# Performance work log

Hardware: AMD Instinct MI355X
Metric: run time of the kernel (lower is better)

Reference implementation:

```python
import jax, jax.numpy as jnp
import numpy as np

NUM_HEADS = 6

def setup_inputs() -> dict:
    key = jax.random.key(0)
    k1, k2, k3, k4 = jax.random.split(key, 4)
    B, N, C = 8, 2048, 384
    x = jax.random.normal(k1, (B, N, C), dtype=jnp.float32)
    qkv_w = jax.random.normal(k2, (3 * C, C), dtype=jnp.float32) * (C ** -0.5)
    proj_w = jax.random.normal(k3, (C, C), dtype=jnp.float32) * (C ** -0.5)
    proj_b = jax.random.normal(k4, (C,), dtype=jnp.float32) * 0.01
    temperature = jnp.ones((NUM_HEADS, 1, 1), dtype=jnp.float32)
    return {"x": x, "qkv_w": qkv_w, "proj_w": proj_w, "proj_b": proj_b,
            "temperature": temperature}


def reference(x, qkv_w, proj_w, proj_b, temperature):
    B, N, C = x.shape
    H = NUM_HEADS
    Dh = C // H
    # qkv projection (no bias), split into q, k, v per head
    qkv = (x @ qkv_w.T).reshape(B, N, 3, H, Dh)
    qkv = jnp.transpose(qkv, (2, 0, 3, 1, 4))  # [3, B, H, N, Dh]
    q, k, v = qkv[0], qkv[1], qkv[2]
    # scores scaled by sqrt(C) (full dim, as in source), then learnable temperature
    attn = jnp.einsum('bhnd,bhmd->bhnm', q, k) / (C ** 0.5)
    attn = attn / temperature  # temperature: [H,1,1] broadcasts over B and N,N
    # diagonal (self-token) mask -> -inf before softmax
    diag = jnp.eye(N, dtype=bool)
    attn = jnp.where(diag, -jnp.inf, attn)
    attn = jax.nn.softmax(attn, axis=-1)
    # attend and merge heads
    out = jnp.einsum('bhnm,bhmd->bhnd', attn, v)
    out = jnp.transpose(out, (0, 2, 1, 3)).reshape(B, N, C)
    # output projection
    return out @ proj_w.T + proj_b
```

## Files before the change

kernel.cpp:

```cpp
#include <hip/hip_runtime.h>


using f32x4 = __attribute__((ext_vector_type(4))) float;
using s16x8 = __attribute__((ext_vector_type(8))) short;
using u16x4 = __attribute__((ext_vector_type(4))) unsigned short;
using u32x2 = __attribute__((ext_vector_type(2))) unsigned int;
using u32x4 = __attribute__((ext_vector_type(4))) unsigned int;
typedef unsigned short u16;
typedef unsigned int u32;

#define MFMA16(a, b, c) __builtin_amdgcn_mfma_f32_16x16x32_bf16(a, b, c, 0, 0, 0)
#define LOG2E 1.4426950408889634f
#define SQRTC 19.595917942265423f

__device__ __forceinline__ u16 f2bf(float f) {
  u32 u = __float_as_uint(f);
  u += 0x7fffu + ((u >> 16) & 1u);
  return (u16)(u >> 16);
}

__device__ __forceinline__ u32 cvtpk(float lo, float hi) {
  u32 r;
  asm("v_cvt_pk_bf16_f32 %0, %1, %2" : "=v"(r) : "v"(lo), "v"(hi));
  return r;
}

__device__ __forceinline__ float fexp2(float x) {
  float r;
  asm("v_exp_f32 %0, %1" : "=v"(r) : "v"(x));
  return r;
}

__device__ __forceinline__ void gld16(const void* g, void* l) {
  __builtin_amdgcn_global_load_lds((const __attribute__((address_space(1))) void*)g,
                                   (__attribute__((address_space(3))) void*)l, 16, 0, 0);
}

__global__ __launch_bounds__(256) void k_cvt2(const float* __restrict__ A,
                                              u16* __restrict__ Oa,
                                              const float* __restrict__ B,
                                              u16* __restrict__ Ob) {
  const int bid = blockIdx.x;
  const float* in;
  u16* out;
  size_t i;
  if (bid < 432) { in = A; out = Oa; i = (size_t)bid * 256 + threadIdx.x; }
  else           { in = B; out = Ob; i = (size_t)(bid - 432) * 256 + threadIdx.x; }
  f32x4 v = *(const f32x4*)(in + i * 4);
  u16x4 o;
  o[0] = f2bf(v[0]); o[1] = f2bf(v[1]); o[2] = f2bf(v[2]); o[3] = f2bf(v[3]);
  *(u16x4*)(out + i * 4) = o;
}

__global__ __launch_bounds__(256) void k_qkv(const float* __restrict__ X,
                                             const u16* __restrict__ W,
                                             const float* __restrict__ temp,
                                             u16* __restrict__ Qt,
                                             u16* __restrict__ Kb,
                                             u16* __restrict__ Vt) {
  __shared__ u16 As[2][128 * 32];
  __shared__ u16 Bs[2][128 * 32];
  const int tid = threadIdx.x, w = tid >> 6, l = tid & 63, lr = l & 15, lg = l >> 4;
  const int id = blockIdx.y * 9 + blockIdx.x;
  const int swz = (id & 7) * 144 + (id >> 3);
  const int tn = (swz % 9) * 128, tm = (swz / 9) * 128;
  const int wr = w >> 1, wc = w & 1;
  const int r0 = tid >> 2, c8 = (tid & 3) * 8;
  const int ar = tid >> 1, ac = (tid & 1) * 16;

  f32x4 acc[4][4] = {};
  f32x4 a4[4];

  auto issueA = [&](int kt) {
    const float* xp = X + (size_t)(tm + ar) * 384 + kt * 32 + ac;
    a4[0] = *(const f32x4*)(xp);
    a4[1] = *(const f32x4*)(xp + 4);
    a4[2] = *(const f32x4*)(xp + 8);
    a4[3] = *(const f32x4*)(xp + 12);
  };
  auto commitA = [&](int buf) {
    u32x4 h0, h1;
    h0[0] = cvtpk(a4[0][0], a4[0][1]); h0[1] = cvtpk(a4[0][2], a4[0][3]);
    h0[2] = cvtpk(a4[1][0], a4[1][1]); h0[3] = cvtpk(a4[1][2], a4[1][3]);
    h1[0] = cvtpk(a4[2][0], a4[2][1]); h1[1] = cvtpk(a4[2][2], a4[2][3]);
    h1[2] = cvtpk(a4[3][0], a4[3][1]); h1[3] = cvtpk(a4[3][2], a4[3][3]);
    *(u32x4*)&As[buf][ar * 32 + ac] = h0;
    *(u32x4*)&As[buf][ar * 32 + ac + 8] = h1;
  };
  auto stageB = [&](int buf, int kt) {
    const int k0 = kt * 32;
    char* db = (char*)(&Bs[buf][0]) + (w << 10);
    gld16(W + (size_t)(tn + r0) * 384 + k0 + c8, db);
    gld16(W + (size_t)(tn + 64 + r0) * 384 + k0 + c8, db + 4096);
  };

  issueA(0); stageB(0, 0); commitA(0);
  for (int kt = 0; kt < 12; ++kt) {
    __syncthreads();
    if (kt < 11) { issueA(kt + 1); stageB((kt + 1) & 1, kt + 1); }
    const int buf = kt & 1;
    s16x8 af[4], bfr[4];
    for (int mi = 0; mi < 4; mi++)
      af[mi] = *(const s16x8*)&As[buf][(wr * 64 + mi * 16 + lr) * 32 + lg * 8];
    for (int ni = 0; ni < 4; ni++)
      bfr[ni] = *(const s16x8*)&Bs[buf][(wc * 64 + ni * 16 + lr) * 32 + lg * 8];
    for (int mi = 0; mi < 4; mi++)
      for (int ni = 0; ni < 4; ni++)
        acc[mi][ni] = MFMA16(af[mi], bfr[ni], acc[mi][ni]);
    if (kt < 11) commitA((kt + 1) & 1);
  }

  const int which = (tn + wc * 64) / 384;
  const int bidx = (tm >> 11);
  for (int mi = 0; mi < 4; mi++)
    for (int ni = 0; ni < 4; ni++) {
      const int n = tn + wc * 64 + ni * 16 + lr;
      const int c = n - which * 384;
      const int h = c >> 6, d = c & 63;
      const size_t bh = (size_t)(bidx * 6 + h);
      if (which == 1) {
        for (int j = 0; j < 4; j++) {
          const int pos = (tm + wr * 64 + mi * 16 + lg * 4 + j) & 2047;
          Kb[(bh * 2048 + pos) * 64 + d] = f2bf(acc[mi][ni][j]);
        }
      } else {
        const float mult = (which == 0) ? (LOG2E / (SQRTC * temp[h])) : 1.0f;
        const int pos0 = (tm + wr * 64 + mi * 16 + lg * 4) & 2047;
        u16x4 vv;
        vv[0] = f2bf(acc[mi][ni][0] * mult); vv[1] = f2bf(acc[mi][ni][1] * mult);
        vv[2] = f2bf(acc[mi][ni][2] * mult); vv[3] = f2bf(acc[mi][ni][3] * mult);
        u16* dst = (which == 0) ? Qt : Vt;
        *(u16x4*)&dst[(bh * 64 + d) * 2048 + pos0] = vv;
      }
    }
}

#define LDSOFF(row, c16) (((row) * 128 + (c16) * 16) ^ (((row) & 7) << 4))

__global__ __launch_bounds__(256, 3) void k_attn(const u16* __restrict__ Qt,
                                                 const u16* __restrict__ Kb,
                                                 const u16* __restrict__ Vt,
                                                 u16* __restrict__ AO) {
  __shared__ u16 Ks[2][64 * 64];
  __shared__ u16 Vs[2][64 * 64];
  __shared__ u16 Ps[4][32 * 72];
  const int tid = threadIdx.x, w = tid >> 6, l = tid & 63, lr = l & 15, lg = l >> 4;
  const int orig = blockIdx.x;
  const int rm = (orig & 7) * 96 + (orig >> 3);
  const int qt = rm & 15, bh = rm >> 4;
  const int h = bh % 6, b = bh / 6;
  const size_t base = (size_t)bh << 17;
  const int q0 = qt * 128 + w * 32;
  const int maskKt = q0 >> 6;
  const int qo = q0 & 63;

  s16x8 qf[2][2];
  for (int mi = 0; mi < 2; mi++)
    for (int ks = 0; ks < 2; ks++) {
      const u16* qp = Qt + base + (size_t)(ks * 32 + lg * 8) * 2048 + q0 + mi * 16 + lr;
      s16x8 q;
      for (int e = 0; e < 8; ++e) q[e] = (short)qp[(size_t)e * 2048];
      qf[mi][ks] = q;
    }

  s16x8 ones;
  for (int e = 0; e < 8; ++e) ones[e] = (short)0x3F80;

  f32x4 o0[4] = {}, o1[4] = {};
  f32x4 os0 = {}, os1 = {};

  const int r0 = tid >> 3, c0 = tid & 7;
  const int c8 = c0 * 8;
  const int wo0 = LDSOFF(r0, c0), wo1 = LDSOFF(r0 + 32, c0);

  s16x8 ka0, ka1, va0, va1;
  auto issue = [&](int kt) {
    const u16* kp = Kb + base + (size_t)(kt * 64 + r0) * 64 + c8;
    ka0 = *(const s16x8*)kp;
    ka1 = *(const s16x8*)(kp + 32 * 64);
    const u16* vp = Vt + base + (size_t)r0 * 2048 + kt * 64 + c8;
    va0 = *(const s16x8*)vp;
    va1 = *(const s16x8*)(vp + 32 * 2048);
  };
  auto commit = [&](int buf) {
    char* kd = (char*)&Ks[buf][0];
    char* vd = (char*)&Vs[buf][0];
    *(s16x8*)(kd + wo0) = ka0; *(s16x8*)(kd + wo1) = ka1;
    *(s16x8*)(vd + wo0) = va0; *(s16x8*)(vd + wo1) = va1;
  };

  issue(0); commit(0);
  __syncthreads();

  const int lrs = (lr & 7) << 4;
  const int x0 = (lg * 16) ^ lrs;
  const int x1 = (64 + lg * 16) ^ lrs;

  for (int kt = 0; kt < 32; ++kt) {
    const int cur = kt & 1;
    if (kt < 31) issue(kt + 1);

    f32x4 st0[4] = {}, st1[4] = {};
    const char* kbp = (const char*)&Ks[cur][0];
    __builtin_amdgcn_s_setprio(1);
    for (int ni = 0; ni < 4; ++ni) {
      const int rb = (ni * 16 + lr) * 128;
      const s16x8 kf0 = *(const s16x8*)(kbp + (rb + x0));
      const s16x8 kf1 = *(const s16x8*)(kbp + (rb + x1));
      st0[ni] = MFMA16(kf0, qf[0][0], st0[ni]);
      st0[ni] = MFMA16(kf1, qf[0][1], st0[ni]);
      st1[ni] = MFMA16(kf0, qf[1][0], st1[ni]);
      st1[ni] = MFMA16(kf1, qf[1][1], st1[ni]);
    }
    __builtin_amdgcn_s_setprio(0);

    if (kt == maskKt) {
      for (int ni = 0; ni < 4; ++ni)
        for (int j = 0; j < 4; ++j) {
          const int kvl = ni * 16 + lg * 4 + j;
          if (kvl == qo + lr)      st0[ni][j] = -1e30f;
          if (kvl == qo + 16 + lr) st1[ni][j] = -1e30f;
        }
    }

    const char* vbp = (const char*)&Vs[cur][0];
    s16x8 vfr[2][4];
    for (int ks = 0; ks < 2; ++ks) {
      const int xk = ks ? x1 : x0;
      for (int dj = 0; dj < 4; ++dj)
        vfr[ks][dj] = *(const s16x8*)(vbp + ((dj * 16 + lr) * 128 + xk));
    }

    u16* const psw = &Ps[w][0];
    {
      u16* pr = psw + lr * 72 + lg * 4;
      for (int ni = 0; ni < 4; ++ni) {
        u32x2 d2;
        d2[0] = cvtpk(fexp2(st0[ni][0]), fexp2(st0[ni][1]));
        d2[1] = cvtpk(fexp2(st0[ni][2]), fexp2(st0[ni][3]));
        *(u32x2*)(pr + ni * 16) = d2;
      }
    }
    {
      const s16x8 pa0k0 = *(const s16x8*)((const char*)(psw + lr * 72) + 0 * 64 + lg * 16);
      const s16x8 pa0k1 = *(const s16x8*)((const char*)(psw + lr * 72) + 1 * 64 + lg * 16);
      __builtin_amdgcn_s_setprio(1);
      for (int dj = 0; dj < 4; ++dj) o0[dj] = MFMA16(pa0k0, vfr[0][dj], o0[dj]);
      os0 = MFMA16(pa0k0, ones, os0);
      for (int dj = 0; dj < 4; ++dj) o0[dj] = MFMA16(pa0k1, vfr[1][dj], o0[dj]);
      os0 = MFMA16(pa0k1, ones, os0);
      __builtin_amdgcn_s_setprio(0);
    }
    {
      u16* pr = psw + (16 + lr) * 72 + lg * 4;
      for (int ni = 0; ni < 4; ++ni) {
        u32x2 d2;
        d2[0] = cvtpk(fexp2(st1[ni][0]), fexp2(st1[ni][1]));
        d2[1] = cvtpk(fexp2(st1[ni][2]), fexp2(st1[ni][3]));
        *(u32x2*)(pr + ni * 16) = d2;
      }
    }
    {
      const s16x8 pa1k0 = *(const s16x8*)((const char*)(psw + (16 + lr) * 72) + 0 * 64 + lg * 16);
      const s16x8 pa1k1 = *(const s16x8*)((const char*)(psw + (16 + lr) * 72) + 1 * 64 + lg * 16);
      __builtin_amdgcn_s_setprio(1);
      for (int dj = 0; dj < 4; ++dj) o1[dj] = MFMA16(pa1k0, vfr[0][dj], o1[dj]);
      os1 = MFMA16(pa1k0, ones, os1);
      for (int dj = 0; dj < 4; ++dj) o1[dj] = MFMA16(pa1k1, vfr[1][dj], o1[dj]);
      os1 = MFMA16(pa1k1, ones, os1);
      __builtin_amdgcn_s_setprio(0);
    }

    if (kt < 31) commit(cur ^ 1);
    __syncthreads();
  }

  f32x4 rv0, rv1;
  for (int j = 0; j < 4; ++j) { rv0[j] = 1.0f / os0[j]; rv1[j] = 1.0f / os1[j]; }
  const size_t aobase = (size_t)b * 2048 * 384 + (size_t)h * 64;
  for (int j = 0; j < 4; ++j) {
    const int pos0 = q0 + lg * 4 + j;
    const int pos1 = pos0 + 16;
    for (int dj = 0; dj < 4; ++dj) {
      AO[aobase + (size_t)pos0 * 384 + dj * 16 + lr] = f2bf(o0[dj][j] * rv0[j]);
      AO[aobase + (size_t)pos1 * 384 + dj * 16 + lr] = f2bf(o1[dj][j] * rv1[j]);
    }
  }
}

__global__ __launch_bounds__(256) void k_proj(const u16* __restrict__ A,
                                              const u16* __restrict__ W,
                                              const float* __restrict__ bias,
                                              float* __restrict__ out) {
  __shared__ u16 As[2][128 * 32];
  __shared__ u16 Bs[2][64 * 32];
  const int tid = threadIdx.x, w = tid >> 6, l = tid & 63, lr = l & 15, lg = l >> 4;
  const int id = blockIdx.y * 6 + blockIdx.x;
  const int swz = (id & 7) * 96 + (id >> 3);
  const int tn = (swz % 6) * 64, tm = (swz / 6) * 128;
  const int r0 = tid >> 2, c8 = (tid & 3) * 8;

  f32x4 acc[2][4] = {};

  auto stage = [&](int buf, int kt) {
    const int k0 = kt * 32;
    char* da = (char*)(&As[buf][0]) + (w << 10);
    char* db = (char*)(&Bs[buf][0]) + (w << 10);
    gld16(A + (size_t)(tm + r0) * 384 + k0 + c8, da);
    gld16(A + (size_t)(tm + 64 + r0) * 384 + k0 + c8, da + 4096);
    gld16(W + (size_t)(tn + r0) * 384 + k0 + c8, db);
  };

  stage(0, 0);
  for (int kt = 0; kt < 12; ++kt) {
    __syncthreads();
    if (kt < 11) stage((kt + 1) & 1, kt + 1);
    const int buf = kt & 1;
    s16x8 af[2], bfr[4];
    for (int mi = 0; mi < 2; mi++)
      af[mi] = *(const s16x8*)&As[buf][(w * 32 + mi * 16 + lr) * 32 + lg * 8];
    for (int ni = 0; ni < 4; ni++)
      bfr[ni] = *(const s16x8*)&Bs[buf][(ni * 16 + lr) * 32 + lg * 8];
    for (int mi = 0; mi < 2; mi++)
      for (int ni = 0; ni < 4; ni++)
        acc[mi][ni] = MFMA16(af[mi], bfr[ni], acc[mi][ni]);
  }

  for (int mi = 0; mi < 2; mi++)
    for (int ni = 0; ni < 4; ni++) {
      const int n = tn + ni * 16 + lr;
      const float bn = bias[n];
      for (int j = 0; j < 4; j++) {
        const int m = tm + w * 32 + mi * 16 + lg * 4 + j;
        out[(size_t)m * 384 + n] = acc[mi][ni][j] + bn;
      }
    }
}

extern "C" void kernel_launch(void* const* d_in, const int* in_sizes, int n_in,
                              void* d_out, int out_size, void* d_ws, size_t ws_size,
                              hipStream_t stream) {
  const float* x      = (const float*)d_in[0];
  const float* qkv_w  = (const float*)d_in[1];
  const float* proj_w = (const float*)d_in[2];
  const float* proj_b = (const float*)d_in[3];
  const float* temp   = (const float*)d_in[4];
  float* out = (float*)d_out;

  u16* wqkvb  = (u16*)d_ws;
  u16* wprojb = wqkvb + 442368;
  u16* Qt     = wprojb + 147456;
  u16* Kb     = Qt + 6291456;
  u16* Vtb    = Kb + 6291456;
  u16* AOb    = Vtb + 6291456;

  k_cvt2<<<576, 256, 0, stream>>>(qkv_w, wqkvb, proj_w, wprojb);
  k_qkv<<<dim3(9, 128), 256, 0, stream>>>(x, wqkvb, temp, Qt, Kb, Vtb);
  k_attn<<<768, 256, 0, stream>>>(Qt, Kb, Vtb, AOb);
  k_proj<<<dim3(6, 128), 256, 0, stream>>>(AOb, wprojb, proj_b, out);
}
```

Measured before the change: 121.8 us.

## Software-pipeline QK with softmax, load V into registers, shuffle row sums

Restructures the attention main loop so the QK^T MFMAs for the next key tile run while the exp/pack and PV work of the current tile proceeds, using ping-pong score registers. K tiles are copied global-to-LDS with a direct load helper, and V fragments are loaded straight from global into registers, removing the V LDS buffer and its commit stores. The softmax denominator is now built from fp32 partial sums reduced with lane shuffles instead of an extra MFMA against a ones vector. The trade-off is higher register pressure and unstaged, less coalesced global reads for V.

```diff
diff --git a/kernel.cpp b/kernel.cpp
--- a/kernel.cpp
+++ b/kernel.cpp
@@ -135,14 +135,11 @@
     }
 }
 
-#define LDSOFF(row, c16) (((row) * 128 + (c16) * 16) ^ (((row) & 7) << 4))
-
 __global__ __launch_bounds__(256, 3) void k_attn(const u16* __restrict__ Qt,
                                                  const u16* __restrict__ Kb,
                                                  const u16* __restrict__ Vt,
                                                  u16* __restrict__ AO) {
   __shared__ u16 Ks[2][64 * 64];
-  __shared__ u16 Vs[2][64 * 64];
   __shared__ u16 Ps[4][32 * 72];
   const int tid = threadIdx.x, w = tid >> 6, l = tid & 63, lr = l & 15, lg = l >> 4;
   const int orig = blockIdx.x;
@@ -163,120 +160,121 @@
       qf[mi][ks] = q;
     }
 
-  s16x8 ones;
-  for (int e = 0; e < 8; ++e) ones[e] = (short)0x3F80;
-
   f32x4 o0[4] = {}, o1[4] = {};
-  f32x4 os0 = {}, os1 = {};
-
-  const int r0 = tid >> 3, c0 = tid & 7;
-  const int c8 = c0 * 8;
-  const int wo0 = LDSOFF(r0, c0), wo1 = LDSOFF(r0 + 32, c0);
-
-  s16x8 ka0, ka1, va0, va1;
-  auto issue = [&](int kt) {
-    const u16* kp = Kb + base + (size_t)(kt * 64 + r0) * 64 + c8;
-    ka0 = *(const s16x8*)kp;
-    ka1 = *(const s16x8*)(kp + 32 * 64);
-    const u16* vp = Vt + base + (size_t)r0 * 2048 + kt * 64 + c8;
-    va0 = *(const s16x8*)vp;
-    va1 = *(const s16x8*)(vp + 32 * 2048);
-  };
-  auto commit = [&](int buf) {
-    char* kd = (char*)&Ks[buf][0];
-    char* vd = (char*)&Vs[buf][0];
-    *(s16x8*)(kd + wo0) = ka0; *(s16x8*)(kd + wo1) = ka1;
-    *(s16x8*)(vd + wo0) = va0; *(s16x8*)(vd + wo1) = va1;
-  };
-
-  issue(0); commit(0);
-  __syncthreads();
+  float sum0 = 0.f, sum1 = 0.f;
+
+  const int kr = w * 8 + (l >> 3);
+  const int kc = (l & 7) ^ (kr & 7);
+  auto gldK = [&](int kt) {
+    const int buf = kt & 1;
+    u16* kd0 = &Ks[buf][0] + w * 512;
+    u16* kd1 = &Ks[buf][2048] + w * 512;
+    gld16(Kb + base + (size_t)(kt * 64 + kr) * 64 + kc * 8, kd0);
+    gld16(Kb + base + (size_t)(kt * 64 + 32 + kr) * 64 + kc * 8, kd1);
+  };
+
+  s16x8 vfr[2][4];
+  auto issueV = [&](int kt) {
+    for (int ks = 0; ks < 2; ++ks)
+      for (int dj = 0; dj < 4; ++dj)
+        vfr[ks][dj] = *(const s16x8*)(Vt + base + (size_t)(dj * 16 + lr) * 2048 +
+                                      kt * 64 + ks * 32 + lg * 8);
+  };
 
   const int lrs = (lr & 7) << 4;
   const int x0 = (lg * 16) ^ lrs;
   const int x1 = (64 + lg * 16) ^ lrs;
 
-  for (int kt = 0; kt < 32; ++kt) {
-    const int cur = kt & 1;
-    if (kt < 31) issue(kt + 1);
-
-    f32x4 st0[4] = {}, st1[4] = {};
-    const char* kbp = (const char*)&Ks[cur][0];
+  auto qk = [&](int kt, f32x4 (&sn0)[4], f32x4 (&sn1)[4]) {
+    const char* kbp = (const char*)&Ks[kt & 1][0];
     __builtin_amdgcn_s_setprio(1);
     for (int ni = 0; ni < 4; ++ni) {
       const int rb = (ni * 16 + lr) * 128;
       const s16x8 kf0 = *(const s16x8*)(kbp + (rb + x0));
       const s16x8 kf1 = *(const s16x8*)(kbp + (rb + x1));
-      st0[ni] = MFMA16(kf0, qf[0][0], st0[ni]);
-      st0[ni] = MFMA16(kf1, qf[0][1], st0[ni]);
-      st1[ni] = MFMA16(kf0, qf[1][0], st1[ni]);
-      st1[ni] = MFMA16(kf1, qf[1][1], st1[ni]);
+      f32x4 z = {};
+      sn0[ni] = MFMA16(kf0, qf[0][0], z);
+      sn0[ni] = MFMA16(kf1, qf[0][1], sn0[ni]);
+      sn1[ni] = MFMA16(kf0, qf[1][0], z);
+      sn1[ni] = MFMA16(kf1, qf[1][1], sn1[ni]);
     }
     __builtin_amdgcn_s_setprio(0);
-
-    if (kt == maskKt) {
-      for (int ni = 0; ni < 4; ++ni)
-        for (int j = 0; j < 4; ++j) {
-          const int kvl = ni * 16 + lg * 4 + j;
-          if (kvl == qo + lr)      st0[ni][j] = -1e30f;
-          if (kvl == qo + 16 + lr) st1[ni][j] = -1e30f;
-        }
-    }
-
-    const char* vbp = (const char*)&Vs[cur][0];
-    s16x8 vfr[2][4];
-    for (int ks = 0; ks < 2; ++ks) {
-      const int xk = ks ? x1 : x0;
-      for (int dj = 0; dj < 4; ++dj)
-        vfr[ks][dj] = *(const s16x8*)(vbp + ((dj * 16 + lr) * 128 + xk));
-    }
-
-    u16* const psw = &Ps[w][0];
-    {
-      u16* pr = psw + lr * 72 + lg * 4;
-      for (int ni = 0; ni < 4; ++ni) {
-        u32x2 d2;
-        d2[0] = cvtpk(fexp2(st0[ni][0]), fexp2(st0[ni][1]));
-        d2[1] = cvtpk(fexp2(st0[ni][2]), fexp2(st0[ni][3]));
-        *(u32x2*)(pr + ni * 16) = d2;
+  };
+
+  u16* const psw = &Ps[w][0];
+  auto packHalf = [&](f32x4 (&st)[4], int rowoff, float& sum) {
+    u16* pr = psw + (rowoff + lr) * 72 + lg * 4;
+    float ls = 0.f;
+    for (int ni = 0; ni < 4; ++ni) {
+      float p0 = fexp2(st[ni][0]), p1 = fexp2(st[ni][1]);
+      float p2 = fexp2(st[ni][2]), p3 = fexp2(st[ni][3]);
+      ls += (p0 + p1) + (p2 + p3);
+      u32x2 d2;
+      d2[0] = cvtpk(p0, p1);
+      d2[1] = cvtpk(p2, p3);
+      *(u32x2*)(pr + ni * 16) = d2;
+    }
+    ls += __shfl_xor(ls, 16);
+    ls += __shfl_xor(ls, 32);
+    sum += ls;
+  };
+  auto maskDiag = [&](f32x4 (&s0)[4], f32x4 (&s1)[4]) {
+    for (int ni = 0; ni < 4; ++ni)
+      for (int j = 0; j < 4; ++j) {
+        const int kvl = ni * 16 + lg * 4 + j;
+        if (kvl == qo + lr)      s0[ni][j] = -1e30f;
+        if (kvl == qo + 16 + lr) s1[ni][j] = -1e30f;
       }
-    }
-    {
-      const s16x8 pa0k0 = *(const s16x8*)((const char*)(psw + lr * 72) + 0 * 64 + lg * 16);
-      const s16x8 pa0k1 = *(const s16x8*)((const char*)(psw + lr * 72) + 1 * 64 + lg * 16);
-      __builtin_amdgcn_s_setprio(1);
-      for (int dj = 0; dj < 4; ++dj) o0[dj] = MFMA16(pa0k0, vfr[0][dj], o0[dj]);
-      os0 = MFMA16(pa0k0, ones, os0);
-      for (int dj = 0; dj < 4; ++dj) o0[dj] = MFMA16(pa0k1, vfr[1][dj], o0[dj]);
-      os0 = MFMA16(pa0k1, ones, os0);
-      __builtin_amdgcn_s_setprio(0);
-    }
-    {
-      u16* pr = psw + (16 + lr) * 72 + lg * 4;
-      for (int ni = 0; ni < 4; ++ni) {
-        u32x2 d2;
-        d2[0] = cvtpk(fexp2(st1[ni][0]), fexp2(st1[ni][1]));
-        d2[1] = cvtpk(fexp2(st1[ni][2]), fexp2(st1[ni][3]));
-        *(u32x2*)(pr + ni * 16) = d2;
-      }
-    }
-    {
-      const s16x8 pa1k0 = *(const s16x8*)((const char*)(psw + (16 + lr) * 72) + 0 * 64 + lg * 16);
-      const s16x8 pa1k1 = *(const s16x8*)((const char*)(psw + (16 + lr) * 72) + 1 * 64 + lg * 16);
-      __builtin_amdgcn_s_setprio(1);
-      for (int dj = 0; dj < 4; ++dj) o1[dj] = MFMA16(pa1k0, vfr[0][dj], o1[dj]);
-      os1 = MFMA16(pa1k0, ones, os1);
-      for (int dj = 0; dj < 4; ++dj) o1[dj] = MFMA16(pa1k1, vfr[1][dj], o1[dj]);
-      os1 = MFMA16(pa1k1, ones, os1);
-      __builtin_amdgcn_s_setprio(0);
-    }
-
-    if (kt < 31) commit(cur ^ 1);
+  };
+  auto pv = [&]() {
+    const s16x8 pa0k0 = *(const s16x8*)((const char*)(psw + lr * 72) + 0 * 64 + lg * 16);
+    const s16x8 pa0k1 = *(const s16x8*)((const char*)(psw + lr * 72) + 1 * 64 + lg * 16);
+    const s16x8 pa1k0 = *(const s16x8*)((const char*)(psw + (16 + lr) * 72) + 0 * 64 + lg * 16);
+    const s16x8 pa1k1 = *(const s16x8*)((const char*)(psw + (16 + lr) * 72) + 1 * 64 + lg * 16);
+    __builtin_amdgcn_s_setprio(1);
+    for (int dj = 0; dj < 4; ++dj) o0[dj] = MFMA16(pa0k0, vfr[0][dj], o0[dj]);
+    for (int dj = 0; dj < 4; ++dj) o0[dj] = MFMA16(pa0k1, vfr[1][dj], o0[dj]);
+    for (int dj = 0; dj < 4; ++dj) o1[dj] = MFMA16(pa1k0, vfr[0][dj], o1[dj]);
+    for (int dj = 0; dj < 4; ++dj) o1[dj] = MFMA16(pa1k1, vfr[1][dj], o1[dj]);
+    __builtin_amdgcn_s_setprio(0);
+  };
+
+  f32x4 stA0[4], stA1[4], stB0[4], stB1[4];
+
+  gldK(0);
+  __syncthreads();
+  issueV(0);
+  gldK(1);
+  qk(0, stA0, stA1);
+  __syncthreads();
+
+  auto body = [&](f32x4 (&sc0)[4], f32x4 (&sc1)[4],
+                  f32x4 (&sn0)[4], f32x4 (&sn1)[4], int t) {
+    if (t < 30) gldK(t + 2);
+    if (t == maskKt) maskDiag(sc0, sc1);
+    packHalf(sc0, 0, sum0);
+    qk(t + 1, sn0, sn1);
+    packHalf(sc1, 16, sum1);
+    pv();
+    issueV(t + 1);
     __syncthreads();
-  }
+  };
+
+  for (int tb = 0; tb < 15; ++tb) {
+    body(stA0, stA1, stB0, stB1, 2 * tb);
+    body(stB0, stB1, stA0, stA1, 2 * tb + 1);
+  }
+  body(stA0, stA1, stB0, stB1, 30);
+  if (31 == maskKt) maskDiag(stB0, stB1);
+  packHalf(stB0, 0, sum0);
+  packHalf(stB1, 16, sum1);
+  pv();
 
   f32x4 rv0, rv1;
-  for (int j = 0; j < 4; ++j) { rv0[j] = 1.0f / os0[j]; rv1[j] = 1.0f / os1[j]; }
+  for (int j = 0; j < 4; ++j) {
+    rv0[j] = 1.0f / __shfl(sum0, lg * 4 + j);
+    rv1[j] = 1.0f / __shfl(sum1, lg * 4 + j);
+  }
   const size_t aobase = (size_t)b * 2048 * 384 + (size_t)h * 64;
   for (int j = 0; j < 4; ++j) {
     const int pos0 = q0 + lg * 4 + j;
```

Measured after the change: 301.5 us. +147.5%, slower.
